# Optimization experiments

Measured on AMD Instinct MI355X. Metric: run time of the kernel, lower is better.

## Reference

```python
import jax, jax.numpy as jnp
import numpy as np

INF = 100000000.0
TOPK = 13
ALPHA = 1
BETA = 6


def box_cxcywh_to_xyxy(b):
    cx, cy, w, h = jnp.split(b, 4, axis=-1)
    return jnp.concatenate([cx - 0.5 * w, cy - 0.5 * h, cx + 0.5 * w, cy + 0.5 * h], axis=-1)


def generalized_box_iou(boxes1, boxes2):
    # boxes1: [N,4] xyxy, boxes2: [G,4] xyxy -> [N,G]
    area1 = (boxes1[:, 2] - boxes1[:, 0]) * (boxes1[:, 3] - boxes1[:, 1])
    area2 = (boxes2[:, 2] - boxes2[:, 0]) * (boxes2[:, 3] - boxes2[:, 1])
    lt = jnp.maximum(boxes1[:, None, :2], boxes2[None, :, :2])
    rb = jnp.minimum(boxes1[:, None, 2:], boxes2[None, :, 2:])
    wh = jnp.clip(rb - lt, 0.0)
    inter = wh[..., 0] * wh[..., 1]
    union = area1[:, None] + area2[None, :] - inter
    iou = inter / union
    lt_e = jnp.minimum(boxes1[:, None, :2], boxes2[None, :, :2])
    rb_e = jnp.maximum(boxes1[:, None, 2:], boxes2[None, :, 2:])
    wh_e = jnp.clip(rb_e - lt_e, 0.0)
    area_e = wh_e[..., 0] * wh_e[..., 1]
    return iou - (area_e - union) / area_e


def _assign_one(cls_logits, bbox_pred, gt_boxes, gt_labels):
    # cls_logits [N,C], bbox_pred [N,4] cxcywh, gt_boxes [G,4] cxcywh, gt_labels [G]
    N = bbox_pred.shape[0]
    G = gt_boxes.shape[0]
    scores = jax.nn.sigmoid(cls_logits)
    overlaps = -generalized_box_iou(box_cxcywh_to_xyxy(bbox_pred), box_cxcywh_to_xyxy(gt_boxes))  # [N,G]
    bbox_scores = scores[:, gt_labels]                       # [N,G] gather per-gt class score
    alignment = bbox_scores ** ALPHA * overlaps ** BETA      # [N,G]
    # per-gt topk over queries
    cand_metrics, cand_idxs = jax.lax.top_k(alignment.T, TOPK)  # [G,K]
    is_pos = cand_metrics > 0
    vals = jnp.take_along_axis(overlaps.T, cand_idxs, axis=1)   # [G,K]
    rows = jnp.broadcast_to(jnp.arange(G)[:, None], (G, TOPK))
    cols = jnp.where(is_pos, cand_idxs, N)  # out-of-bounds col -> dropped
    oinf = jnp.full((G, N), -INF, dtype=overlaps.dtype)
    oinf = oinf.at[rows, cols].set(vals, mode='drop')
    max_overlaps = oinf.max(axis=0)     # [N]
    argmax_overlaps = oinf.argmax(axis=0)
    pos = max_overlaps != -INF
    assigned_gt_inds = jnp.where(pos, argmax_overlaps + 1, 0)
    assign_metrics = jnp.where(pos, alignment[jnp.arange(N), argmax_overlaps], 0.0)
    assigned_labels = jnp.where(pos, gt_labels[argmax_overlaps], -1)
    return assigned_gt_inds, assigned_labels, assign_metrics


def setup_inputs() -> dict:
    key = jax.random.key(0)
    k1, k2, k3, k4 = jax.random.split(key, 4)
    bs, N, C, G = 16, 4000, 80, 300
    return {
        'pred_logits': jax.random.normal(k1, (bs, N, C), dtype=jnp.float32),
        'pred_boxes': jax.random.uniform(k2, (bs, N, 4), dtype=jnp.float32, minval=0.05, maxval=0.95),
        'gt_boxes': jax.random.uniform(k3, (bs, G, 4), dtype=jnp.float32, minval=0.05, maxval=0.95),
        'gt_labels': jax.random.randint(k4, (bs, G), 0, C),
    }


def reference(pred_logits, pred_boxes, gt_boxes, gt_labels):
    # Fixed-shape equivalent of matched_list: assigned_gt_inds[b,q] == 0 means
    # background; k>0 means query q matched to gt k-1 (same semantics as the
    # (valid_query_idx, valid_assigned_gt_inds) pairs in the torch code).
    return jax.vmap(_assign_one)(pred_logits, pred_boxes, gt_boxes, gt_labels)
```

## Files before the change

kernel.cpp:

```cpp
#include <hip/hip_runtime.h>

#define NPRED  4000
#define NGROUP 1000
#define NGT    300
#define NCLS   80
#define TOPKK  13
#define NCHUNK 63

typedef unsigned long long u64;

__device__ __forceinline__ float frcp(float x) { return __builtin_amdgcn_rcpf(x); }
__device__ __forceinline__ float fexp(float x) {
    return __builtin_amdgcn_exp2f(x * 1.44269504088896341f);
}

__device__ __forceinline__ float neg_giou_x(float4 p, float gx1, float gy1,
                                            float gx2, float gy2, float garea) {
    float pa  = (p.z - p.x) * (p.w - p.y);
    float whx = fmaxf(fminf(p.z, gx2) - fmaxf(p.x, gx1), 0.0f);
    float why = fmaxf(fminf(p.w, gy2) - fmaxf(p.y, gy1), 0.0f);
    float inter = whx * why;
    float uni = pa + garea - inter;
    float iou = inter * frcp(uni);
    float wex = fmaxf(p.z, gx2) - fminf(p.x, gx1);
    float wey = fmaxf(p.w, gy2) - fminf(p.y, gy1);
    float area_e = wex * wey;
    return (area_e - uni) * frcp(area_e) - iou;
}

__device__ __forceinline__ float4 to_xyxy(float4 pb) {
    return make_float4(pb.x - 0.5f * pb.z, pb.y - 0.5f * pb.w,
                       pb.x + 0.5f * pb.z, pb.y + 0.5f * pb.w);
}

__device__ __forceinline__ float sigmoid_fast(float x) {
    return frcp(1.0f + fexp(-x));
}

__device__ __forceinline__ float pow6(float x) {
    float x2 = x * x;
    float x4 = x2 * x2;
    return x2 * x4;
}

__device__ __forceinline__ unsigned ord_float(float f) {
    unsigned u = __float_as_uint(f);
    return u ^ ((unsigned)(((int)u) >> 31) | 0x80000000u);
}

__device__ __forceinline__ u64 pack_key(float v, int n) {
    return ((u64)__float_as_uint(v) << 32) | (u64)(~(unsigned)n);
}

__global__ void init_keys(u64* keys, int n) {
    int i = blockIdx.x * blockDim.x + threadIdx.x;
    if (i < n) keys[i] = 0ULL;
}

__global__ __launch_bounds__(256) void sig_transpose(const float* __restrict__ logits,
                                                     const float4* __restrict__ pboxes,
                                                     float* __restrict__ st,
                                                     float4* __restrict__ pxyxy,
                                                     u64* __restrict__ keys,
                                                     int total_keys) {
    const int tid = threadIdx.x;
    const int gid = blockIdx.x * 256 + tid;
    if (gid < total_keys) keys[gid] = 0ULL;

    const int b = blockIdx.x / NCHUNK;
    const int n0 = (blockIdx.x % NCHUNK) * 64;
    const int nval = (NPRED - n0 < 64) ? (NPRED - n0) : 64;

    if (tid < 64 && tid < nval) {
        pxyxy[(size_t)b * NPRED + n0 + tid] =
            to_xyxy(pboxes[(size_t)b * NPRED + n0 + tid]);
    }

    __shared__ float tile[NCLS][64 + 1];

    const float4* src = (const float4*)(logits + ((size_t)b * NPRED + n0) * NCLS);
    #pragma unroll
    for (int it = 0; it < 5; ++it) {
        int i4 = tid + it * 256;
        int p = i4 / 20;
        int c = i4 * 4 - p * 80;
        if (p < nval) {
            float4 v = src[i4];
            tile[c + 0][p] = sigmoid_fast(v.x);
            tile[c + 1][p] = sigmoid_fast(v.y);
            tile[c + 2][p] = sigmoid_fast(v.z);
            tile[c + 3][p] = sigmoid_fast(v.w);
        }
    }
    __syncthreads();
    float* dstbase = st + (size_t)b * NCLS * NPRED + n0;
    #pragma unroll
    for (int it = 0; it < 5; ++it) {
        int w4 = tid + it * 256;
        int c = w4 >> 4, r4 = (w4 & 15) * 4;
        if (r4 < nval) {
            float4 v = make_float4(tile[c][r4], tile[c][r4 + 1],
                                   tile[c][r4 + 2], tile[c][r4 + 3]);
            *(float4*)(dstbase + (size_t)c * NPRED + r4) = v;
        }
    }
}

template <bool PRE>
__global__ __launch_bounds__(256) void topk_scatter(const float* __restrict__ logits,
                                                    const float* __restrict__ st,
                                                    const float4* __restrict__ pboxes,
                                                    const float4* __restrict__ pxyxy,
                                                    const float4* __restrict__ gboxes,
                                                    const int* __restrict__ glabels,
                                                    u64* __restrict__ keys) {
    const int blk = blockIdx.x;
    const int b = blk / NGT;
    const int g = blk - b * NGT;
    const int tid = threadIdx.x;
    const int wave = tid >> 6;
    const int lane = tid & 63;

    __shared__ __align__(16) float s_key[NPRED];
    __shared__ u64 s_pair[2][8];
    __shared__ u64 s_win[TOPKK];

    float4 gb = gboxes[b * NGT + g];
    const int lab = glabels[b * NGT + g];
    const float gx1 = gb.x - 0.5f * gb.z;
    const float gy1 = gb.y - 0.5f * gb.w;
    const float gx2 = gb.x + 0.5f * gb.z;
    const float gy2 = gb.y + 0.5f * gb.w;
    const float garea = (gx2 - gx1) * (gy2 - gy1);

    const float* lg = logits + (size_t)b * NPRED * NCLS + lab;
    const float* srow = st + ((size_t)b * NCLS + lab) * NPRED;
    const float4* srow4 = (const float4*)srow;
    const float4* pbb = pboxes + (size_t)b * NPRED;
    const float4* pxr = pxyxy + (size_t)b * NPRED;

    u64 b1 = 0ULL, b2 = 0ULL;
    #pragma unroll
    for (int j = 0; j < 4; ++j) {
        int grp = tid + j * 256;
        if (grp < NGROUP) {
            int n0 = grp * 4;
            float s0, s1, s2, s3;
            float4 p0, p1, p2, p3;
            if (PRE) {
                float4 s4 = srow4[grp];
                s0 = s4.x; s1 = s4.y; s2 = s4.z; s3 = s4.w;
                p0 = pxr[n0]; p1 = pxr[n0 + 1]; p2 = pxr[n0 + 2]; p3 = pxr[n0 + 3];
            } else {
                s0 = sigmoid_fast(lg[(size_t)(n0 + 0) * NCLS]);
                s1 = sigmoid_fast(lg[(size_t)(n0 + 1) * NCLS]);
                s2 = sigmoid_fast(lg[(size_t)(n0 + 2) * NCLS]);
                s3 = sigmoid_fast(lg[(size_t)(n0 + 3) * NCLS]);
                p0 = to_xyxy(pbb[n0]);     p1 = to_xyxy(pbb[n0 + 1]);
                p2 = to_xyxy(pbb[n0 + 2]); p3 = to_xyxy(pbb[n0 + 3]);
            }
            float v0 = s0 * pow6(neg_giou_x(p0, gx1, gy1, gx2, gy2, garea));
            float v1 = s1 * pow6(neg_giou_x(p1, gx1, gy1, gx2, gy2, garea));
            float v2 = s2 * pow6(neg_giou_x(p2, gx1, gy1, gx2, gy2, garea));
            float v3 = s3 * pow6(neg_giou_x(p3, gx1, gy1, gx2, gy2, garea));
            *(float4*)&s_key[n0] = make_float4(v0, v1, v2, v3);
            u64 k0 = pack_key(v0, n0);
            u64 k1 = pack_key(v1, n0 + 1);
            u64 k2 = pack_key(v2, n0 + 2);
            u64 k3 = pack_key(v3, n0 + 3);
            if (k0 > b1)      { b2 = b1; b1 = k0; } else if (k0 > b2) b2 = k0;
            if (k1 > b1)      { b2 = b1; b1 = k1; } else if (k1 > b2) b2 = k1;
            if (k2 > b1)      { b2 = b1; b1 = k2; } else if (k2 > b2) b2 = k2;
            if (k3 > b1)      { b2 = b1; b1 = k3; } else if (k3 > b2) b2 = k3;
        }
    }

    int nwin = 0;
    for (int k = 0; k < 7; ++k) {
        u64 m1 = b1, m2 = b2;
        #pragma unroll
        for (int m = 1; m < 64; m <<= 1) {
            u64 o1 = __shfl_xor(m1, m, 64);
            u64 o2 = __shfl_xor(m2, m, 64);
            u64 hi = (m1 > o1) ? m1 : o1;
            u64 lo = (m1 > o1) ? o1 : m1;
            u64 c2 = (m2 > o2) ? m2 : o2;
            m2 = (lo > c2) ? lo : c2;
            m1 = hi;
        }
        const int buf = k & 1;
        if (lane == 0) { s_pair[buf][wave * 2] = m1; s_pair[buf][wave * 2 + 1] = m2; }
        __syncthreads();
        u64 t1 = 0ULL, t2 = 0ULL;
        #pragma unroll
        for (int w = 0; w < 8; ++w) {
            u64 c = s_pair[buf][w];
            if (c > t1)      { t2 = t1; t1 = c; }
            else if (c > t2) { t2 = c; }
        }
        bool p1 = (unsigned)(t1 >> 32) != 0u;
        if (!p1) break;
        bool p2 = ((unsigned)(t2 >> 32) != 0u) && (2 * k + 1 < TOPKK);
        if (tid == 0) {
            s_win[2 * k] = t1;
            if (p2) s_win[2 * k + 1] = t2;
        }
        nwin = 2 * k + 1 + (p2 ? 1 : 0);
        if (!p2 || 2 * k + 1 == TOPKK - 1) {
            if (!p2) break;
        }
        int n1 = (int)(~(unsigned)t1);
        int n2 = p2 ? (int)(~(unsigned)t2) : -1;
        bool own1 = (((n1 >> 2) & 255) == tid);
        bool own2 = p2 && (((n2 >> 2) & 255) == tid);
        if (own1 | own2) {
            if (own1) s_key[n1] = 0.0f;
            if (own2) s_key[n2] = 0.0f;
            if (own1 && own2) {
                b1 = 0ULL; b2 = 0ULL;
            } else if (b2 != 0ULL) {
                b1 = b2; b2 = 0ULL;
            } else {
                b1 = 0ULL;
            }
            if (b1 == 0ULL) {
                #pragma unroll
                for (int jj = 0; jj < 4; ++jj) {
                    int grp = tid + jj * 256;
                    if (grp >= NGROUP) continue;
                    int n0 = grp * 4;
                    float4 q = *(const float4*)&s_key[n0];
                    u64 c0 = pack_key(q.x, n0);
                    u64 c1 = pack_key(q.y, n0 + 1);
                    u64 c2k = pack_key(q.z, n0 + 2);
                    u64 c3 = pack_key(q.w, n0 + 3);
                    if (c0 > b1)      { b2 = b1; b1 = c0; } else if (c0 > b2) b2 = c0;
                    if (c1 > b1)      { b2 = b1; b1 = c1; } else if (c1 > b2) b2 = c1;
                    if (c2k > b1)     { b2 = b1; b1 = c2k; } else if (c2k > b2) b2 = c2k;
                    if (c3 > b1)      { b2 = b1; b1 = c3; } else if (c3 > b2) b2 = c3;
                }
            }
        }
    }
    __syncthreads();

    if (tid < nwin) {
        u64 t = s_win[tid];
        int wi = (int)(~(unsigned)t);
        float o;
        if (PRE) {
            o = neg_giou_x(pxr[wi], gx1, gy1, gx2, gy2, garea);
        } else {
            o = neg_giou_x(to_xyxy(pbb[wi]), gx1, gy1, gx2, gy2, garea);
        }
        unsigned mbits = (unsigned)(t >> 32) >> 16;
        u64 key = ((u64)ord_float(o) << 32)
                | ((u64)(511u - (unsigned)g) << 23)
                | ((u64)mbits << 7);
        atomicMax(&keys[(size_t)b * NPRED + wi], key);
    }
}

__global__ void finalize(const int* __restrict__ glabels,
                         const u64* __restrict__ keys,
                         float* __restrict__ out, int total) {
    int i = blockIdx.x * blockDim.x + threadIdx.x;
    if (i >= total) return;
    int b = i / NPRED;
    u64 key = keys[i];
    float o0 = 0.0f, o1 = -1.0f, o2 = 0.0f;
    if (key != 0ULL) {
        int g = 511 - (int)((key >> 23) & 0x1FF);
        o0 = (float)(g + 1);
        o1 = (float)glabels[b * NGT + g];
        o2 = __uint_as_float(((unsigned)(key >> 7) & 0xFFFFu) << 16);
    }
    out[i] = o0;
    out[(size_t)total + i] = o1;
    out[(size_t)2 * total + i] = o2;
}

extern "C" void kernel_launch(void* const* d_in, const int* in_sizes, int n_in,
                              void* d_out, int out_size, void* d_ws, size_t ws_size,
                              hipStream_t stream) {
    const float* logits  = (const float*)d_in[0];
    const float4* pboxes = (const float4*)d_in[1];
    const float4* gboxes = (const float4*)d_in[2];
    const int* glabels   = (const int*)d_in[3];

    const int bs = in_sizes[3] / NGT;
    const int total = bs * NPRED;
    char* ws = (char*)d_ws;
    u64* keys   = (u64*)ws;                    ws += (size_t)total * 8;
    float* st   = (float*)ws;                  ws += (size_t)bs * NCLS * NPRED * 4;
    float4* pxy = (float4*)ws;                 ws += (size_t)total * 16;
    float* out = (float*)d_out;

    const size_t need = (size_t)(ws - (char*)d_ws);
    if (ws_size >= need) {
        sig_transpose<<<bs * NCHUNK, 256, 0, stream>>>(logits, pboxes, st, pxy,
                                                       keys, total);
        topk_scatter<true><<<bs * NGT, 256, 0, stream>>>(logits, st, pboxes, pxy,
                                                         gboxes, glabels, keys);
    } else {
        init_keys<<<(total + 255) / 256, 256, 0, stream>>>(keys, total);
        topk_scatter<false><<<bs * NGT, 256, 0, stream>>>(logits, st, pboxes, pxy,
                                                          gboxes, glabels, keys);
    }
    finalize<<<(total + 255) / 256, 256, 0, stream>>>(glabels, keys, out, total);
}
```

Measured before the change: 140.8 us.

## Extract top-k one winner per round, re-reducing only the owner wave

The per-gt top-k selection now extracts one winner per iteration instead of two. Only the wave that owned the removed element redoes its 64-lane shuffle reduction, while the other waves keep their cached per-wave maxima in shared memory. This is meant to cut the shuffle and cross-wave reduction work per round, at the cost of up to 13 barrier rounds instead of 7. Separately, the sigmoid/transpose prep kernel now works on 32-query chunks instead of 64, launching more, smaller blocks with less shared memory each.

```diff
diff --git a/kernel.cpp b/kernel.cpp
--- a/kernel.cpp
+++ b/kernel.cpp
@@ -5,7 +5,7 @@
 #define NGT    300
 #define NCLS   80
 #define TOPKK  13
-#define NCHUNK 63
+#define NCHUNK 125
 
 typedef unsigned long long u64;
 
@@ -68,23 +68,22 @@
     if (gid < total_keys) keys[gid] = 0ULL;
 
     const int b = blockIdx.x / NCHUNK;
-    const int n0 = (blockIdx.x % NCHUNK) * 64;
-    const int nval = (NPRED - n0 < 64) ? (NPRED - n0) : 64;
-
-    if (tid < 64 && tid < nval) {
+    const int n0 = (blockIdx.x % NCHUNK) * 32;
+
+    if (tid < 32) {
         pxyxy[(size_t)b * NPRED + n0 + tid] =
             to_xyxy(pboxes[(size_t)b * NPRED + n0 + tid]);
     }
 
-    __shared__ float tile[NCLS][64 + 1];
+    __shared__ float tile[NCLS][32 + 1];
 
     const float4* src = (const float4*)(logits + ((size_t)b * NPRED + n0) * NCLS);
     #pragma unroll
-    for (int it = 0; it < 5; ++it) {
+    for (int it = 0; it < 3; ++it) {
         int i4 = tid + it * 256;
-        int p = i4 / 20;
-        int c = i4 * 4 - p * 80;
-        if (p < nval) {
+        if (i4 < 640) {
+            int p = i4 / 20;
+            int c = (i4 - p * 20) * 4;
             float4 v = src[i4];
             tile[c + 0][p] = sigmoid_fast(v.x);
             tile[c + 1][p] = sigmoid_fast(v.y);
@@ -95,10 +94,10 @@
     __syncthreads();
     float* dstbase = st + (size_t)b * NCLS * NPRED + n0;
     #pragma unroll
-    for (int it = 0; it < 5; ++it) {
+    for (int it = 0; it < 3; ++it) {
         int w4 = tid + it * 256;
-        int c = w4 >> 4, r4 = (w4 & 15) * 4;
-        if (r4 < nval) {
+        if (w4 < 640) {
+            int c = w4 >> 3, r4 = (w4 & 7) * 4;
             float4 v = make_float4(tile[c][r4], tile[c][r4 + 1],
                                    tile[c][r4 + 2], tile[c][r4 + 3]);
             *(float4*)(dstbase + (size_t)c * NPRED + r4) = v;
@@ -122,7 +121,7 @@
     const int lane = tid & 63;
 
     __shared__ __align__(16) float s_key[NPRED];
-    __shared__ u64 s_pair[2][8];
+    __shared__ u64 s_wave[4];
     __shared__ u64 s_win[TOPKK];
 
     float4 gb = gboxes[b * NGT + g];
@@ -168,62 +167,41 @@
             u64 k1 = pack_key(v1, n0 + 1);
             u64 k2 = pack_key(v2, n0 + 2);
             u64 k3 = pack_key(v3, n0 + 3);
-            if (k0 > b1)      { b2 = b1; b1 = k0; } else if (k0 > b2) b2 = k0;
-            if (k1 > b1)      { b2 = b1; b1 = k1; } else if (k1 > b2) b2 = k1;
-            if (k2 > b1)      { b2 = b1; b1 = k2; } else if (k2 > b2) b2 = k2;
-            if (k3 > b1)      { b2 = b1; b1 = k3; } else if (k3 > b2) b2 = k3;
-        }
-    }
-
-    int nwin = 0;
-    for (int k = 0; k < 7; ++k) {
-        u64 m1 = b1, m2 = b2;
+            if (k0 > b1) { b2 = b1; b1 = k0; } else if (k0 > b2) b2 = k0;
+            if (k1 > b1) { b2 = b1; b1 = k1; } else if (k1 > b2) b2 = k1;
+            if (k2 > b1) { b2 = b1; b1 = k2; } else if (k2 > b2) b2 = k2;
+            if (k3 > b1) { b2 = b1; b1 = k3; } else if (k3 > b2) b2 = k3;
+        }
+    }
+
+    {
+        u64 m1 = b1;
         #pragma unroll
         for (int m = 1; m < 64; m <<= 1) {
-            u64 o1 = __shfl_xor(m1, m, 64);
-            u64 o2 = __shfl_xor(m2, m, 64);
-            u64 hi = (m1 > o1) ? m1 : o1;
-            u64 lo = (m1 > o1) ? o1 : m1;
-            u64 c2 = (m2 > o2) ? m2 : o2;
-            m2 = (lo > c2) ? lo : c2;
-            m1 = hi;
-        }
-        const int buf = k & 1;
-        if (lane == 0) { s_pair[buf][wave * 2] = m1; s_pair[buf][wave * 2 + 1] = m2; }
+            u64 o = __shfl_xor(m1, m, 64);
+            if (o > m1) m1 = o;
+        }
+        if (lane == 0) s_wave[wave] = m1;
+    }
+
+    int nwin = 0;
+    for (int k = 0; k < TOPKK; ++k) {
         __syncthreads();
-        u64 t1 = 0ULL, t2 = 0ULL;
-        #pragma unroll
-        for (int w = 0; w < 8; ++w) {
-            u64 c = s_pair[buf][w];
-            if (c > t1)      { t2 = t1; t1 = c; }
-            else if (c > t2) { t2 = c; }
-        }
-        bool p1 = (unsigned)(t1 >> 32) != 0u;
-        if (!p1) break;
-        bool p2 = ((unsigned)(t2 >> 32) != 0u) && (2 * k + 1 < TOPKK);
-        if (tid == 0) {
-            s_win[2 * k] = t1;
-            if (p2) s_win[2 * k + 1] = t2;
-        }
-        nwin = 2 * k + 1 + (p2 ? 1 : 0);
-        if (!p2 || 2 * k + 1 == TOPKK - 1) {
-            if (!p2) break;
-        }
+        u64 t1 = s_wave[0];
+        u64 c;
+        c = s_wave[1]; if (c > t1) t1 = c;
+        c = s_wave[2]; if (c > t1) t1 = c;
+        c = s_wave[3]; if (c > t1) t1 = c;
+        if ((unsigned)(t1 >> 32) == 0u) break;
+        if (tid == 0) s_win[k] = t1;
+        nwin = k + 1;
         int n1 = (int)(~(unsigned)t1);
-        int n2 = p2 ? (int)(~(unsigned)t2) : -1;
-        bool own1 = (((n1 >> 2) & 255) == tid);
-        bool own2 = p2 && (((n2 >> 2) & 255) == tid);
-        if (own1 | own2) {
-            if (own1) s_key[n1] = 0.0f;
-            if (own2) s_key[n2] = 0.0f;
-            if (own1 && own2) {
-                b1 = 0ULL; b2 = 0ULL;
-            } else if (b2 != 0ULL) {
-                b1 = b2; b2 = 0ULL;
-            } else {
+        int ownerTid = (n1 >> 2) & 255;
+        if (tid == ownerTid) {
+            s_key[n1] = 0.0f;
+            if (b2 != 0ULL) { b1 = b2; b2 = 0ULL; }
+            else {
                 b1 = 0ULL;
-            }
-            if (b1 == 0ULL) {
                 #pragma unroll
                 for (int jj = 0; jj < 4; ++jj) {
                     int grp = tid + jj * 256;
@@ -232,14 +210,23 @@
                     float4 q = *(const float4*)&s_key[n0];
                     u64 c0 = pack_key(q.x, n0);
                     u64 c1 = pack_key(q.y, n0 + 1);
-                    u64 c2k = pack_key(q.z, n0 + 2);
+                    u64 c2 = pack_key(q.z, n0 + 2);
                     u64 c3 = pack_key(q.w, n0 + 3);
-                    if (c0 > b1)      { b2 = b1; b1 = c0; } else if (c0 > b2) b2 = c0;
-                    if (c1 > b1)      { b2 = b1; b1 = c1; } else if (c1 > b2) b2 = c1;
-                    if (c2k > b1)     { b2 = b1; b1 = c2k; } else if (c2k > b2) b2 = c2k;
-                    if (c3 > b1)      { b2 = b1; b1 = c3; } else if (c3 > b2) b2 = c3;
+                    if (c0 > b1) { b2 = b1; b1 = c0; } else if (c0 > b2) b2 = c0;
+                    if (c1 > b1) { b2 = b1; b1 = c1; } else if (c1 > b2) b2 = c1;
+                    if (c2 > b1) { b2 = b1; b1 = c2; } else if (c2 > b2) b2 = c2;
+                    if (c3 > b1) { b2 = b1; b1 = c3; } else if (c3 > b2) b2 = c3;
                 }
             }
+        }
+        if ((ownerTid >> 6) == wave) {
+            u64 m1 = b1;
+            #pragma unroll
+            for (int m = 1; m < 64; m <<= 1) {
+                u64 o = __shfl_xor(m1, m, 64);
+                if (o > m1) m1 = o;
+            }
+            if (lane == 0) s_wave[wave] = m1;
         }
     }
     __syncthreads();
```

Result: faster. 123.4 us (median of 3 runs) (-12.4%).
